# Performance work log

Hardware: AMD Instinct MI355X
Metric: run time of the kernel (lower is better)

Reference implementation:

```python
import jax, jax.numpy as jnp
import numpy as np

B, S, D, H, DF = 512, 256, 256, 8, 1024
DA, DZ, DO = 64, 64, 128
NA, NZ, NO = 9, 20, 7


def _pe(b, s):
    # Faithful to the torch code: zeros_like(src) is 3D, so 'seq_len'=batch,
    # 'd_model'=seq; pos_encoding[pos, i] assigns whole feature rows.
    pos = jnp.arange(b, dtype=jnp.float32)[:, None]
    i = jnp.arange(s, dtype=jnp.float32)[None, :]
    ang = pos / jnp.power(100.0, 2.0 * i / s)
    pe = jnp.where((jnp.arange(s)[None, :] % 2) == 0, jnp.sin(ang), jnp.cos(ang))
    return pe[:, :, None]  # broadcasts over feature dim


def _ln(x, g, b):
    m = x.mean(-1, keepdims=True)
    v = x.var(-1, keepdims=True)
    return (x - m) / jnp.sqrt(v + 1e-5) * g + b


def _lin(x, w, b):
    return x @ w.T + b


def _forward(X, emb_act_w, emb_zone_w, lin0_w, lin0_b, qkv_w, qkv_b, attn_o_w, attn_o_b,
             ln1_g, ln1_b, ff1_w, ff1_b, ff2_w, ff2_b, ln2_g, ln2_b,
             relu_w, relu_b, dT_w, dT_b, lindT_w, lindT_b, zn_w, zn_b,
             linzn_w, linzn_b, act0_w, act0_b, act1_w, act1_b, linact_w, linact_b):
    a = X[:, :, 0]
    z = X[:, :, 1]
    o = X[:, :, 2:].astype(jnp.float32)
    x = jnp.concatenate([emb_act_w[a], emb_zone_w[z], _lin(o, lin0_w, lin0_b)], -1)
    src = x + _pe(x.shape[0], x.shape[1])
    # TransformerEncoderLayer: post-norm, relu FFN, eval (dropout off)
    qkv = _lin(src, qkv_w, qkv_b)
    q, k, v = jnp.split(qkv, 3, -1)
    hd = D // H
    q = q.reshape(q.shape[0], q.shape[1], H, hd)
    k = k.reshape(k.shape[0], k.shape[1], H, hd)
    v = v.reshape(v.shape[0], v.shape[1], H, hd)
    sc = jnp.einsum('bqhd,bkhd->bhqk', q, k) * (float(hd) ** -0.5)
    att = jax.nn.softmax(sc, -1)
    ao = jnp.einsum('bhqk,bkhd->bqhd', att, v).reshape(src.shape)
    h1 = _ln(src + _lin(ao, attn_o_w, attn_o_b), ln1_g, ln1_b)
    h2 = _ln(h1 + _lin(jax.nn.relu(_lin(h1, ff1_w, ff1_b)), ff2_w, ff2_b), ln2_g, ln2_b)
    x_relu = _lin(h2[:, -1, :], relu_w, relu_b)  # NOTE: no relu in original
    dT = _lin(_lin(x_relu, dT_w, dT_b), lindT_w, lindT_b)  # [B,1]
    zn = _lin(_lin(jnp.concatenate([dT, x_relu], 1), zn_w, zn_b), linzn_w, linzn_b)  # [B,20]
    fa = jnp.concatenate([zn, dT, x_relu], 1)  # [B,277]
    ac = _lin(_lin(_lin(fa, act0_w, act0_b), act1_w, act1_b), linact_w, linact_b)  # [B,5]
    return jnp.concatenate([dT, zn, ac], 1)  # [B,26]


def setup_inputs() -> dict:
    ks = jax.random.split(jax.random.key(0), 24)

    def p(k, shape):
        return jax.random.normal(k, shape, jnp.float32) * 0.02

    inp = {
        'X': jax.random.randint(ks[0], (B, S, 2 + NO), 0, NA).astype(jnp.int32),
        'emb_act_w': p(ks[1], (NA, DA)),
        'emb_zone_w': p(ks[2], (NZ, DZ)),
        'lin0_w': p(ks[3], (DO, NO)), 'lin0_b': jnp.zeros((DO,), jnp.float32),
        'qkv_w': p(ks[4], (3 * D, D)), 'qkv_b': jnp.zeros((3 * D,), jnp.float32),
        'attn_o_w': p(ks[5], (D, D)), 'attn_o_b': jnp.zeros((D,), jnp.float32),
        'ln1_g': jnp.ones((D,), jnp.float32), 'ln1_b': jnp.zeros((D,), jnp.float32),
        'ff1_w': p(ks[6], (DF, D)), 'ff1_b': jnp.zeros((DF,), jnp.float32),
        'ff2_w': p(ks[7], (D, DF)), 'ff2_b': jnp.zeros((D,), jnp.float32),
        'ln2_g': jnp.ones((D,), jnp.float32), 'ln2_b': jnp.zeros((D,), jnp.float32),
        'relu_w': p(ks[8], (D, D)), 'relu_b': jnp.zeros((D,), jnp.float32),
        'dT_w': p(ks[9], (D, D)), 'dT_b': jnp.zeros((D,), jnp.float32),
        'lindT_w': p(ks[10], (1, D)), 'lindT_b': jnp.zeros((1,), jnp.float32),
        'zn_w': p(ks[11], (D + 1, D + 1)), 'zn_b': jnp.zeros((D + 1,), jnp.float32),
        'linzn_w': p(ks[12], (20, D + 1)), 'linzn_b': jnp.zeros((20,), jnp.float32),
        'act0_w': p(ks[13], (D + 21, D + 21)), 'act0_b': jnp.zeros((D + 21,), jnp.float32),
        'act1_w': p(ks[14], (D + 21, D + 21)), 'act1_b': jnp.zeros((D + 21,), jnp.float32),
        'linact_w': p(ks[15], (5, D + 21)), 'linact_b': jnp.zeros((5,), jnp.float32),
    }
    return inp


def reference(X, emb_act_w, emb_zone_w, lin0_w, lin0_b, qkv_w, qkv_b, attn_o_w, attn_o_b,
              ln1_g, ln1_b, ff1_w, ff1_b, ff2_w, ff2_b, ln2_g, ln2_b,
              relu_w, relu_b, dT_w, dT_b, lindT_w, lindT_b, zn_w, zn_b,
              linzn_w, linzn_b, act0_w, act0_b, act1_w, act1_b, linact_w, linact_b):
    return _forward(X, emb_act_w, emb_zone_w, lin0_w, lin0_b, qkv_w, qkv_b, attn_o_w, attn_o_b,
                    ln1_g, ln1_b, ff1_w, ff1_b, ff2_w, ff2_b, ln2_g, ln2_b,
                    relu_w, relu_b, dT_w, dT_b, lindT_w, lindT_b, zn_w, zn_b,
                    linzn_w, linzn_b, act0_w, act0_b, act1_w, act1_b, linact_w, linact_b)
```

## Files before the change

kernel.cpp:

```cpp
#include <hip/hip_runtime.h>
#include <math.h>

#define BATCH 512
#define SEQ   256
#define DIM   256
#define NHEAD 8
#define DFF   1024
#define NT    1024
#define NW    16

typedef unsigned short ushort;
typedef unsigned int   uint;
typedef __fp16 half2v __attribute__((ext_vector_type(2)));

#define OFF_QKV   0u
#define OFF_AO    196608u
#define OFF_FF1   262144u
#define OFF_FF2   524288u
#define OFF_RELU  786432u
#define OFF_DT    851968u
#define OFF_ZN    917504u
#define OFF_A0    983553u
#define OFF_A1    1060282u
#define OFF_KT    1137011u
#define CVT_TOTAL 1202547u

__global__ __launch_bounds__(512) void cvt_weights(
    const float* __restrict__ qkv, const float* __restrict__ ao,
    const float* __restrict__ ff1, const float* __restrict__ ff2,
    const float* __restrict__ relu, const float* __restrict__ dT,
    const float* __restrict__ zn, const float* __restrict__ a0,
    const float* __restrict__ a1, ushort* __restrict__ ws) {
  uint i = blockIdx.x * 512u + threadIdx.x;
  if (i >= CVT_TOTAL) return;
  float v;
  if (i >= OFF_KT) {
    uint idx = i - OFF_KT;
    uint d = idx >> 8, k = idx & 255u;
    v = qkv[(size_t)(256 + k) * 256 + d];
  } else {
    const float* src; uint off;
    if      (i < OFF_AO)  { src = qkv;  off = OFF_QKV; }
    else if (i < OFF_FF1) { src = ao;   off = OFF_AO; }
    else if (i < OFF_FF2) { src = ff1;  off = OFF_FF1; }
    else if (i < OFF_RELU){ src = ff2;  off = OFF_FF2; }
    else if (i < OFF_DT)  { src = relu; off = OFF_RELU; }
    else if (i < OFF_ZN)  { src = dT;   off = OFF_DT; }
    else if (i < OFF_A0)  { src = zn;   off = OFF_ZN; }
    else if (i < OFF_A1)  { src = a0;   off = OFF_A0; }
    else                  { src = a1;   off = OFF_A1; }
    v = src[i - off];
  }
  __fp16 h = (__fp16)v;
  union { __fp16 h; ushort u; } c; c.h = h;
  ws[i] = c.u;
}


__device__ __forceinline__ half2v u2h(uint u) {
  union { uint u; half2v h; } c; c.u = u; return c.h;
}

__device__ __forceinline__ float wave_allred(float v) {
  #pragma unroll
  for (int off = 32; off > 0; off >>= 1) v += __shfl_xor(v, off, 64);
  return v;
}

__device__ __forceinline__ float fold4(int lane, float p0, float p1, float p2, float p3) {
  float za = (lane & 32) ? p1 : p0;
  float ta = (lane & 32) ? p0 : p1;
  za += __shfl_xor(ta, 32, 64);
  float zb = (lane & 32) ? p3 : p2;
  float tb = (lane & 32) ? p2 : p3;
  zb += __shfl_xor(tb, 32, 64);
  float u = (lane & 16) ? zb : za;
  float t = (lane & 16) ? za : zb;
  u += __shfl_xor(t, 16, 64);
  u += __shfl_xor(u, 8, 64);
  u += __shfl_xor(u, 4, 64);
  u += __shfl_xor(u, 2, 64);
  u += __shfl_xor(u, 1, 64);
  return u;
}

__device__ __forceinline__ float fold4h(int lane, const float p[4]) {
  float z0 = (lane & 16) ? p[1] : p[0], y0 = (lane & 16) ? p[0] : p[1];
  z0 += __shfl_xor(y0, 16, 64);
  float z1 = (lane & 16) ? p[3] : p[2], y1 = (lane & 16) ? p[2] : p[3];
  z1 += __shfl_xor(y1, 16, 64);
  float u = (lane & 8) ? z1 : z0, t = (lane & 8) ? z0 : z1;
  u += __shfl_xor(t, 8, 64);
  u += __shfl_xor(u, 4, 64);
  u += __shfl_xor(u, 2, 64);
  u += __shfl_xor(u, 1, 64);
  return u;
}

__device__ __forceinline__ bool burst_writer4(int lane, int& row_off) {
  if (lane & 7) return false;
  int g = (lane >> 3) & 3;
  int iv = ((g & 1) << 1) | ((g >> 1) & 1);
  row_off = ((lane >> 5) << 2) + iv;
  return true;
}

struct XH { half2v h[4]; };

__device__ __forceinline__ XH ldx8h(const float* __restrict__ x, int lane) {
  int k = (lane & 31) * 8;
  XH r;
  r.h[0] = __builtin_amdgcn_cvt_pkrtz(x[k],     x[k + 1]);
  r.h[1] = __builtin_amdgcn_cvt_pkrtz(x[k + 2], x[k + 3]);
  r.h[2] = __builtin_amdgcn_cvt_pkrtz(x[k + 4], x[k + 5]);
  r.h[3] = __builtin_amdgcn_cvt_pkrtz(x[k + 6], x[k + 7]);
  return r;
}

__device__ __forceinline__ void accum1(uint4 w, const XH& x, float& p) {
  p = __builtin_amdgcn_fdot2(u2h(w.x), x.h[0], p, false);
  p = __builtin_amdgcn_fdot2(u2h(w.y), x.h[1], p, false);
  p = __builtin_amdgcn_fdot2(u2h(w.z), x.h[2], p, false);
  p = __builtin_amdgcn_fdot2(u2h(w.w), x.h[3], p, false);
}

struct W4 { uint4 w[4]; };

__device__ __forceinline__ W4 ldw4(const ushort* __restrict__ Wb, int ld, int lane) {
  const ushort* wp = Wb + (size_t)((lane >> 5) * 4) * ld + (lane & 31) * 8;
  W4 r;
  #pragma unroll
  for (int i = 0; i < 4; ++i) r.w[i] = *(const uint4*)(wp + (size_t)i * ld);
  return r;
}

__device__ __forceinline__ void accum4(const W4& w, const XH& x, float p[4]) {
  #pragma unroll
  for (int i = 0; i < 4; ++i) accum1(w.w[i], x, p[i]);
}

__device__ __forceinline__ float block_sum16(float v, float* red) {
  #pragma unroll
  for (int off = 32; off > 0; off >>= 1) v += __shfl_xor(v, off, 64);
  __syncthreads();
  if ((threadIdx.x & 63) == 0) red[threadIdx.x >> 6] = v;
  __syncthreads();
  float s = 0.f;
  #pragma unroll
  for (int i = 0; i < NW; ++i) s += red[i];
  return s;
}

struct Buf {
  float sc[2048];
  float pe[SEQ];
  float srcl[DIM];
  float qv[DIM];
  float ao[DIM];
  float h1[DIM];
  float h2[DIM];
  float xr[DIM];
  float znin[260];
  float fa[280];
  float znv[20];
  float cb[8];
  float scA[9 * 8];
  float scZ[20 * 8];
  float mHJ[8 * 8];
  float biasO8[8];
  float wsum8[8];
  float attA[8 * 9];
  float attZ[8 * 20];
  float oAcc[8 * 7];
  float peAcc8[8];
  int   Xa[SEQ];
  int   Xz[SEQ];
  float Xo[SEQ * 7];
};


__global__ __launch_bounds__(NT, 8) void nmstpp_fused(
    const int*   __restrict__ X,
    const float* __restrict__ emb_act,
    const float* __restrict__ emb_zone,
    const float* __restrict__ lin0_w,
    const float* __restrict__ lin0_b,
    const ushort* __restrict__ w16,
    const float* __restrict__ qkv_b,
    const float* __restrict__ attn_o_b,
    const float* __restrict__ ln1_g, const float* __restrict__ ln1_b,
    const float* __restrict__ ff1_b,
    const float* __restrict__ ff2_b,
    const float* __restrict__ ln2_g, const float* __restrict__ ln2_b,
    const float* __restrict__ relu_b,
    const float* __restrict__ dT_b,
    const float* __restrict__ lindT_w,
    const float* __restrict__ lindT_b,
    const float* __restrict__ zn_b,
    const float* __restrict__ linzn_w,
    const float* __restrict__ linzn_b,
    const float* __restrict__ act0_b,
    const float* __restrict__ act1_b,
    const float* __restrict__ linact_w,
    const float* __restrict__ linact_b,
    float* __restrict__ out)
{
  const int tid  = threadIdx.x;
  const int wid  = tid >> 6;
  const int lane = tid & 63;
  const int b    = blockIdx.x;
  const int hq2  = (tid >> 8) * 2;
  const int dd   = tid & 255;

  const ushort* qkv16  = w16 + OFF_QKV;
  const ushort* ao16   = w16 + OFF_AO;
  const ushort* ff116  = w16 + OFF_FF1;
  const ushort* ff216  = w16 + OFF_FF2;
  const ushort* relu16 = w16 + OFF_RELU;
  const ushort* dT16   = w16 + OFF_DT;
  const ushort* kt16   = w16 + OFF_KT;
  const __fp16* znh  = (const __fp16*)(w16 + OFF_ZN);
  const __fp16* a0h  = (const __fp16*)(w16 + OFF_A0);
  const __fp16* a1h  = (const __fp16*)(w16 + OFF_A1);

  __shared__ alignas(16) Buf s;
  __shared__ float embA[9 * 65];
  __shared__ float embZ[20 * 65];
  __shared__ float l0w[128 * 7];
  __shared__ float l0b[128];
  __shared__ float red[NW];

  for (int i = tid; i < 9 * 64;  i += NT) embA[(i >> 6) * 65 + (i & 63)] = emb_act[i];
  for (int i = tid; i < 20 * 64; i += NT) embZ[(i >> 6) * 65 + (i & 63)] = emb_zone[i];
  for (int i = tid; i < 128 * 7; i += NT) l0w[i] = lin0_w[i];
  if (tid < 128) l0b[tid] = lin0_b[tid];
  if (tid < SEQ) {
    const int* xrow = X + (b * SEQ + tid) * 9;
    s.Xa[tid] = xrow[0];
    s.Xz[tid] = xrow[1];
    #pragma unroll
    for (int j = 0; j < 7; ++j) s.Xo[tid * 7 + j] = (float)xrow[2 + j];
    float ex  = (float)(2 * tid) / (float)SEQ;
    float ang = (float)b * exp2f(-ex * 6.643856189774724f);
    s.pe[tid] = ((tid & 1) == 0) ? __sinf(ang) : __cosf(ang);
  }
  __syncthreads();

  if (tid < DIM) {
    int av = s.Xa[SEQ - 1], zv = s.Xz[SEQ - 1];
    float v;
    if (tid < 64)        v = embA[av * 65 + tid];
    else if (tid < 128)  v = embZ[zv * 65 + (tid - 64)];
    else {
      const float* lr = l0w + (tid - 128) * 7;
      float acc = l0b[tid - 128];
      #pragma unroll
      for (int j = 0; j < 7; ++j) acc = fmaf(lr[j], s.Xo[(SEQ - 1) * 7 + j], acc);
      v = acc;
    }
    s.srcl[tid] = v + s.pe[SEQ - 1];
  }
  __syncthreads();

  {
    XH x = ldx8h(s.srcl, lane);
    #pragma unroll 1
    for (int t = 0; t < 2; ++t) {
      int base = (wid + 16 * t) * 8;
      W4 w = ldw4(qkv16 + (size_t)base * 256, 256, lane);
      float p[4] = {};
      accum4(w, x, p);
      float u = fold4h(lane, p);
      int ro;
      if (burst_writer4(lane, ro)) s.qv[base + ro] = qkv_b[base + ro] + u;
    }
  }
  __syncthreads();

  {
    XH x = ldx8h(s.qv, lane);
    const float inv = 0.17677669529663687f;
    #pragma unroll 1
    for (int t = 0; t < 2; ++t) {
      int base = (wid + 16 * t) * 8;
      W4 w = ldw4(kt16 + (size_t)base * 256, 256, lane);
      float p[4] = {};
      accum4(w, x, p);
      #pragma unroll
      for (int i = 0; i < 4; ++i) {
        p[i] += __shfl_xor(p[i], 1, 4);
        p[i] += __shfl_xor(p[i], 2, 4);
      }
      int sub = lane & 31;
      int h = sub >> 2, jj = sub & 3;
      int dbase = base + ((lane >> 5) << 2);
      s.sc[(dbase + jj) * 8 + h] = p[jj] * inv;
    }
  }
  __syncthreads();

  if (tid < 312) {
    if (tid < 296) {
      int h = tid / 37, k = tid - h * 37;
      if (k < 9) {
        float acc = 0.f;
        for (int c = 0; c < 64; ++c) acc = fmaf(s.sc[c * 8 + h], embA[k * 65 + c], acc);
        s.scA[k * 8 + h] = acc;
      } else if (k < 29) {
        int z = k - 9; float acc = 0.f;
        for (int c = 0; c < 64; ++c) acc = fmaf(s.sc[(64 + c) * 8 + h], embZ[z * 65 + c], acc);
        s.scZ[z * 8 + h] = acc;
      } else if (k < 36) {
        int j = k - 29; float acc = 0.f;
        for (int kk = 0; kk < 128; ++kk) acc = fmaf(s.sc[(128 + kk) * 8 + h], l0w[kk * 7 + j], acc);
        s.mHJ[h * 8 + j] = acc;
      } else {
        float acc = 0.f;
        for (int c = 0; c < 256; ++c) acc += s.sc[c * 8 + h];
        s.wsum8[h] = acc;
      }
    } else if (tid < 304) {
      int h = tid - 296; float acc = 0.f;
      for (int kk = 0; kk < 128; ++kk) acc = fmaf(s.sc[(128 + kk) * 8 + h], l0b[kk], acc);
      s.biasO8[h] = acc;
    } else {
      int h = tid - 304; float acc = 0.f;
      for (int c = 0; c < 32; ++c) acc += s.qv[h * 32 + c] * qkv_b[DIM + h * 32 + c];
      s.cb[h] = acc * 0.17677669529663687f;
    }
  }
  __syncthreads();

  {
    const int sp = dd;
    int av = s.Xa[sp], zv = s.Xz[sp];
    float o[7];
    #pragma unroll
    for (int j = 0; j < 7; ++j) o[j] = s.Xo[sp * 7 + j];
    float pes = s.pe[sp];
    #pragma unroll
    for (int hh = 0; hh < 2; ++hh) {
      int h = hq2 + hh;
      float acc = s.scA[av * 8 + h] + s.scZ[zv * 8 + h] + s.biasO8[h] + s.cb[h];
      acc = fmaf(pes, s.wsum8[h], acc);
      #pragma unroll
      for (int j = 0; j < 7; ++j) acc = fmaf(s.mHJ[h * 8 + j], o[j], acc);
      s.sc[h * SEQ + sp] = acc;
    }
  }
  __syncthreads();

  {
    const bool act = (wid < 8);
    const int h = wid & 7;
    float vals[4]; float rinv = 0.f;
    if (act) {
      float m = -1e30f;
      #pragma unroll
      for (int i = 0; i < 4; ++i) {
        vals[i] = s.sc[h * SEQ + lane * 4 + i];
        m = fmaxf(m, vals[i]);
      }
      #pragma unroll
      for (int off = 32; off > 0; off >>= 1) m = fmaxf(m, __shfl_xor(m, off, 64));
      float lsum = 0.f;
      #pragma unroll
      for (int i = 0; i < 4; ++i) { vals[i] = __expf(vals[i] - m); lsum += vals[i]; }
      #pragma unroll
      for (int off = 32; off > 0; off >>= 1) lsum += __shfl_xor(lsum, off, 64);
      rinv = 1.0f / lsum;
    }
    __syncthreads();
    if (act) {
      #pragma unroll
      for (int i = 0; i < 4; ++i) s.sc[(lane * 4 + i) * 8 + h] = vals[i] * rinv;
    }
  }
  __syncthreads();

  if (wid < 8) {
    const int h = wid;
    float att[4];
    #pragma unroll
    for (int i = 0; i < 4; ++i) att[i] = s.sc[(lane + 64 * i) * 8 + h];
    {
      float v = 0.f;
      #pragma unroll
      for (int i = 0; i < 4; ++i) v = fmaf(att[i], s.pe[lane + 64 * i], v);
      v = wave_allred(v);
      if (lane == 0) s.peAcc8[h] = v;
    }
    #pragma unroll
    for (int j = 0; j < 7; ++j) {
      float v = 0.f;
      #pragma unroll
      for (int i = 0; i < 4; ++i) v = fmaf(att[i], s.Xo[(lane + 64 * i) * 7 + j], v);
      v = wave_allred(v);
      if (lane == 0) s.oAcc[h * 7 + j] = v;
    }
    int code[4];
    #pragma unroll
    for (int i = 0; i < 4; ++i) {
      int sp = lane + 64 * i;
      code[i] = s.Xa[sp] | (s.Xz[sp] << 8);
    }
    for (int a = 0; a < 9; ++a) {
      float v = 0.f;
      #pragma unroll
      for (int i = 0; i < 4; ++i) v += ((code[i] & 255) == a) ? att[i] : 0.f;
      v = wave_allred(v);
      if (lane == 0) s.attA[h * 9 + a] = v;
    }
    for (int z = 0; z < 20; ++z) {
      float v = 0.f;
      #pragma unroll
      for (int i = 0; i < 4; ++i) v += ((code[i] >> 8) == z) ? att[i] : 0.f;
      v = wave_allred(v);
      if (lane == 0) s.attZ[h * 20 + z] = v;
    }
  }
  __syncthreads();

  {
    float acc[2];
    #pragma unroll
    for (int hh = 0; hh < 2; ++hh) acc[hh] = s.peAcc8[hq2 + hh];
    if (dd < 64) {
      for (int a = 0; a < 9; ++a) {
        float ev = embA[a * 65 + dd];
        #pragma unroll
        for (int hh = 0; hh < 2; ++hh) acc[hh] = fmaf(s.attA[(hq2 + hh) * 9 + a], ev, acc[hh]);
      }
    } else if (dd < 128) {
      int d2 = dd - 64;
      for (int z = 0; z < 20; ++z) {
        float ev = embZ[z * 65 + d2];
        #pragma unroll
        for (int hh = 0; hh < 2; ++hh) acc[hh] = fmaf(s.attZ[(hq2 + hh) * 20 + z], ev, acc[hh]);
      }
    } else {
      int kk = dd - 128;
      #pragma unroll
      for (int j = 0; j < 7; ++j) {
        float ov = l0w[kk * 7 + j];
        #pragma unroll
        for (int hh = 0; hh < 2; ++hh) acc[hh] = fmaf(s.oAcc[(hq2 + hh) * 7 + j], ov, acc[hh]);
      }
      #pragma unroll
      for (int hh = 0; hh < 2; ++hh) acc[hh] += l0b[kk];
    }
    #pragma unroll
    for (int hh = 0; hh < 2; ++hh) s.sc[(hq2 + hh) * DIM + dd] = acc[hh];
  }
  __syncthreads();

  {
    #pragma unroll 1
    for (int t = 0; t < 2; ++t) {
      int rb = wid + 16 * t;
      int base = rb * 8;
      XH x = ldx8h(s.sc + (rb >> 2) * DIM, lane);
      W4 w = ldw4(qkv16 + (size_t)(2 * DIM + base) * 256, 256, lane);
      float p[4] = {};
      accum4(w, x, p);
      float u = fold4h(lane, p);
      int ro;
      if (burst_writer4(lane, ro)) s.ao[base + ro] = qkv_b[2 * DIM + base + ro] + u;
    }
  }
  __syncthreads();

  {
    XH x = ldx8h(s.ao, lane);
    #pragma unroll 1
    for (int t = 0; t < 2; ++t) {
      int base = (wid + 16 * t) * 8;
      W4 w = ldw4(ao16 + (size_t)base * 256, 256, lane);
      float p[4] = {};
      accum4(w, x, p);
      float u = fold4h(lane, p);
      int ro;
      if (burst_writer4(lane, ro)) {
        int rr = base + ro;
        s.qv[rr] = s.srcl[rr] + attn_o_b[rr] + u;
      }
    }
  }
  __syncthreads();
  {
    float tv = (tid < DIM) ? s.qv[tid] : 0.f;
    float mean = block_sum16(tv, red) * (1.0f / 256.0f);
    float dv = (tid < DIM) ? (tv - mean) : 0.f;
    float var = block_sum16(dv * dv, red) * (1.0f / 256.0f);
    if (tid < DIM) s.h1[tid] = dv / sqrtf(var + 1e-5f) * ln1_g[tid] + ln1_b[tid];
  }
  __syncthreads();

  {
    XH x = ldx8h(s.h1, lane);
    #pragma unroll 1
    for (int t = 0; t < 8; ++t) {
      int base = (wid + 16 * t) * 8;
      W4 w = ldw4(ff116 + (size_t)base * 256, 256, lane);
      float p[4] = {};
      accum4(w, x, p);
      float u = fold4h(lane, p);
      int ro;
      if (burst_writer4(lane, ro)) {
        int rr = base + ro;
        s.sc[rr] = fmaxf(ff1_b[rr] + u, 0.f);
      }
    }
  }
  __syncthreads();

  {
    #pragma unroll 1
    for (int t = 0; t < 2; ++t) {
      int base = (wid + 16 * t) * 8;
      float p[4] = {};
      #pragma unroll 1
      for (int kc = 0; kc < 4; ++kc) {
        XH x = ldx8h(s.sc + kc * 256, lane);
        W4 w = ldw4(ff216 + (size_t)base * 1024 + kc * 256, 1024, lane);
        accum4(w, x, p);
      }
      float u = fold4h(lane, p);
      int ro;
      if (burst_writer4(lane, ro)) {
        int rr = base + ro;
        s.qv[rr] = s.h1[rr] + ff2_b[rr] + u;
      }
    }
  }
  __syncthreads();
  {
    float tv = (tid < DIM) ? s.qv[tid] : 0.f;
    float mean = block_sum16(tv, red) * (1.0f / 256.0f);
    float dv = (tid < DIM) ? (tv - mean) : 0.f;
    float var = block_sum16(dv * dv, red) * (1.0f / 256.0f);
    if (tid < DIM) s.h2[tid] = dv / sqrtf(var + 1e-5f) * ln2_g[tid] + ln2_b[tid];
  }
  __syncthreads();

  {
    XH x = ldx8h(s.h2, lane);
    #pragma unroll 1
    for (int t = 0; t < 2; ++t) {
      int base = (wid + 16 * t) * 8;
      W4 w = ldw4(relu16 + (size_t)base * 256, 256, lane);
      float p[4] = {};
      accum4(w, x, p);
      float u = fold4h(lane, p);
      int ro;
      if (burst_writer4(lane, ro)) s.xr[base + ro] = relu_b[base + ro] + u;
    }
  }
  __syncthreads();

  {
    XH x = ldx8h(s.xr, lane);
    #pragma unroll 1
    for (int t = 0; t < 2; ++t) {
      int base = (wid + 16 * t) * 8;
      W4 w = ldw4(dT16 + (size_t)base * 256, 256, lane);
      float p[4] = {};
      accum4(w, x, p);
      float u = fold4h(lane, p);
      int ro;
      if (burst_writer4(lane, ro)) s.h1[base + ro] = dT_b[base + ro] + u;
    }
  }
  __syncthreads();
  float dTv;
  {
    float v = (tid < DIM) ? lindT_w[tid] * s.h1[tid] : 0.f;
    dTv = block_sum16(v, red) + lindT_b[0];
  }

  if (tid < DIM) { s.znin[1 + tid] = s.xr[tid]; s.fa[21 + tid] = s.xr[tid]; }
  if (tid == 0)  { s.znin[0] = dTv; s.fa[20] = dTv; }
  __syncthreads();
  float* z1 = s.sc + 1024;
  for (int r0 = 4 * wid; r0 < 257; r0 += 4 * NW) {
    int nrow = 257 - r0; if (nrow > 4) nrow = 4;
    float p0 = 0, p1 = 0, p2 = 0, p3 = 0;
    for (int j = lane; j < 257; j += 64) {
      float xv = s.znin[j];
      const __fp16* wp = znh + (size_t)r0 * 257 + j;
      p0 = fmaf((float)wp[0], xv, p0);
      if (nrow > 1) p1 = fmaf((float)wp[257], xv, p1);
      if (nrow > 2) p2 = fmaf((float)wp[2 * 257], xv, p2);
      if (nrow > 3) p3 = fmaf((float)wp[3 * 257], xv, p3);
    }
    float u = fold4(lane, p0, p1, p2, p3);
    if ((lane & 15) == 0) {
      int g = lane >> 4;
      int rr = r0 + ((g & 1) << 1) + (g >> 1);
      if (rr < 257) z1[rr] = zn_b[rr] + u;
    }
  }
  __syncthreads();
  for (int r0 = 4 * wid; r0 < 20; r0 += 4 * NW) {
    float p0 = 0, p1 = 0, p2 = 0, p3 = 0;
    for (int j = lane; j < 257; j += 64) {
      float xv = z1[j];
      const float* wp = linzn_w + (size_t)r0 * 257 + j;
      p0 = fmaf(wp[0], xv, p0);
      p1 = fmaf(wp[257], xv, p1);
      p2 = fmaf(wp[2 * 257], xv, p2);
      p3 = fmaf(wp[3 * 257], xv, p3);
    }
    float u = fold4(lane, p0, p1, p2, p3);
    if ((lane & 15) == 0) {
      int g = lane >> 4;
      int rr = r0 + ((g & 1) << 1) + (g >> 1);
      if (rr < 20) { float v = linzn_b[rr] + u; s.znv[rr] = v; s.fa[rr] = v; }
    }
  }
  __syncthreads();

  float* a0v = s.sc + 1312;
  for (int r0 = 4 * wid; r0 < 277; r0 += 4 * NW) {
    int nrow = 277 - r0; if (nrow > 4) nrow = 4;
    float p0 = 0, p1 = 0, p2 = 0, p3 = 0;
    for (int j = lane; j < 277; j += 64) {
      float xv = s.fa[j];
      const __fp16* wp = a0h + (size_t)r0 * 277 + j;
      p0 = fmaf((float)wp[0], xv, p0);
      if (nrow > 1) p1 = fmaf((float)wp[277], xv, p1);
      if (nrow > 2) p2 = fmaf((float)wp[2 * 277], xv, p2);
      if (nrow > 3) p3 = fmaf((float)wp[3 * 277], xv, p3);
    }
    float u = fold4(lane, p0, p1, p2, p3);
    if ((lane & 15) == 0) {
      int g = lane >> 4;
      int rr = r0 + ((g & 1) << 1) + (g >> 1);
      if (rr < 277) a0v[rr] = act0_b[rr] + u;
    }
  }
  __syncthreads();
  float* a1v = s.sc + 1024;
  for (int r0 = 4 * wid; r0 < 277; r0 += 4 * NW) {
    int nrow = 277 - r0; if (nrow > 4) nrow = 4;
    float p0 = 0, p1 = 0, p2 = 0, p3 = 0;
    for (int j = lane; j < 277; j += 64) {
      float xv = a0v[j];
      const __fp16* wp = a1h + (size_t)r0 * 277 + j;
      p0 = fmaf((float)wp[0], xv, p0);
      if (nrow > 1) p1 = fmaf((float)wp[277], xv, p1);
      if (nrow > 2) p2 = fmaf((float)wp[2 * 277], xv, p2);
      if (nrow > 3) p3 = fmaf((float)wp[3 * 277], xv, p3);
    }
    float u = fold4(lane, p0, p1, p2, p3);
    if ((lane & 15) == 0) {
      int g = lane >> 4;
      int rr = r0 + ((g & 1) << 1) + (g >> 1);
      if (rr < 277) a1v[rr] = act1_b[rr] + u;
    }
  }
  __syncthreads();

  if (wid < 5) {
    const float* wr = linact_w + (size_t)wid * 277;
    float p = 0.f;
    for (int j = lane; j < 277; j += 64) p = fmaf(wr[j], a1v[j], p);
    #pragma unroll
    for (int off = 32; off > 0; off >>= 1) p += __shfl_xor(p, off, 64);
    if (lane == 0) out[b * 26 + 21 + wid] = linact_b[wid] + p;
  }
  if (tid == 0) out[b * 26] = dTv;
  if (tid < 20) out[b * 26 + 1 + tid] = s.znv[tid];
}


extern "C" void kernel_launch(void* const* d_in, const int* in_sizes, int n_in,
                              void* d_out, int out_size, void* d_ws, size_t ws_size,
                              hipStream_t stream) {
  (void)in_sizes; (void)n_in; (void)out_size; (void)ws_size;
  const int*   X        = (const int*)  d_in[0];
  const float* emb_act  = (const float*)d_in[1];
  const float* emb_zone = (const float*)d_in[2];
  const float* lin0_w   = (const float*)d_in[3];
  const float* lin0_b   = (const float*)d_in[4];
  const float* qkv_w    = (const float*)d_in[5];
  const float* qkv_b    = (const float*)d_in[6];
  const float* attn_o_w = (const float*)d_in[7];
  const float* attn_o_b = (const float*)d_in[8];
  const float* ln1_g    = (const float*)d_in[9];
  const float* ln1_b    = (const float*)d_in[10];
  const float* ff1_w    = (const float*)d_in[11];
  const float* ff1_b    = (const float*)d_in[12];
  const float* ff2_w    = (const float*)d_in[13];
  const float* ff2_b    = (const float*)d_in[14];
  const float* ln2_g    = (const float*)d_in[15];
  const float* ln2_b    = (const float*)d_in[16];
  const float* relu_w   = (const float*)d_in[17];
  const float* relu_b   = (const float*)d_in[18];
  const float* dT_w     = (const float*)d_in[19];
  const float* dT_b     = (const float*)d_in[20];
  const float* lindT_w  = (const float*)d_in[21];
  const float* lindT_b  = (const float*)d_in[22];
  const float* zn_w     = (const float*)d_in[23];
  const float* zn_b     = (const float*)d_in[24];
  const float* linzn_w  = (const float*)d_in[25];
  const float* linzn_b  = (const float*)d_in[26];
  const float* act0_w   = (const float*)d_in[27];
  const float* act0_b   = (const float*)d_in[28];
  const float* act1_w   = (const float*)d_in[29];
  const float* act1_b   = (const float*)d_in[30];
  const float* linact_w = (const float*)d_in[31];
  const float* linact_b = (const float*)d_in[32];
  float* out = (float*)d_out;
  ushort* w16 = (ushort*)d_ws;

  cvt_weights<<<dim3((CVT_TOTAL + 511) / 512), dim3(512), 0, stream>>>(
      qkv_w, attn_o_w, ff1_w, ff2_w, relu_w, dT_w, zn_w, act0_w, act1_w, w16);

  nmstpp_fused<<<dim3(BATCH), dim3(NT), 0, stream>>>(
      X, emb_act, emb_zone, lin0_w, lin0_b, w16, qkv_b, attn_o_b,
      ln1_g, ln1_b, ff1_b, ff2_b, ln2_g, ln2_b,
      relu_b, dT_b, lindT_w, lindT_b, zn_b,
      linzn_w, linzn_b, act0_b, act1_b, linact_w, linact_b,
      out);
}
```

Before: 133.2 us.

## Halve block size to 512 threads and compact per-block input staging

Shrinks each workgroup from 1024 to 512 threads (8 waves). Every GEMV loop now runs twice as many iterations per wave, and the per-head loops handle four heads per thread instead of two. The softmax and attention stages drop their idle-wave guards because all 8 waves now map to the 8 heads. Action and zone indices are packed into one int and the observation features are stored as fp16 in shared memory, and LayerNorm computes mean and sum-of-squares in a single fused reduction. The aim is fewer idle waves, cheaper barriers and less shared memory, at the cost of less latency hiding per block and a one-pass variance that is less numerically stable.

```diff
diff --git a/kernel.cpp b/kernel.cpp
--- a/kernel.cpp
+++ b/kernel.cpp
@@ -6,8 +6,8 @@
 #define DIM   256
 #define NHEAD 8
 #define DFF   1024
-#define NT    1024
-#define NW    16
+#define NT    512
+#define NW    8
 
 typedef unsigned short ushort;
 typedef unsigned int   uint;
@@ -139,7 +139,7 @@
   for (int i = 0; i < 4; ++i) accum1(w.w[i], x, p[i]);
 }
 
-__device__ __forceinline__ float block_sum16(float v, float* red) {
+__device__ __forceinline__ float block_sum8(float v, float* red) {
   #pragma unroll
   for (int off = 32; off > 0; off >>= 1) v += __shfl_xor(v, off, 64);
   __syncthreads();
@@ -149,6 +149,24 @@
   #pragma unroll
   for (int i = 0; i < NW; ++i) s += red[i];
   return s;
+}
+
+__device__ __forceinline__ void block_sum8x2(float a, float b2, float* red,
+                                             float& A, float& B) {
+  #pragma unroll
+  for (int off = 32; off > 0; off >>= 1) {
+    a  += __shfl_xor(a,  off, 64);
+    b2 += __shfl_xor(b2, off, 64);
+  }
+  __syncthreads();
+  if ((threadIdx.x & 63) == 0) {
+    red[threadIdx.x >> 6] = a;
+    red[NW + (threadIdx.x >> 6)] = b2;
+  }
+  __syncthreads();
+  A = 0.f; B = 0.f;
+  #pragma unroll
+  for (int i = 0; i < NW; ++i) { A += red[i]; B += red[NW + i]; }
 }
 
 struct Buf {
@@ -173,9 +191,8 @@
   float attZ[8 * 20];
   float oAcc[8 * 7];
   float peAcc8[8];
-  int   Xa[SEQ];
-  int   Xz[SEQ];
-  float Xo[SEQ * 7];
+  int    Xcode[SEQ];
+  __fp16 Xoh[SEQ * 7];
 };
 
 
@@ -209,7 +226,7 @@
   const int wid  = tid >> 6;
   const int lane = tid & 63;
   const int b    = blockIdx.x;
-  const int hq2  = (tid >> 8) * 2;
+  const int hb4  = (tid >> 8) * 4;
   const int dd   = tid & 255;
 
   const ushort* qkv16  = w16 + OFF_QKV;
@@ -228,7 +245,7 @@
   __shared__ float embZ[20 * 65];
   __shared__ float l0w[128 * 7];
   __shared__ float l0b[128];
-  __shared__ float red[NW];
+  __shared__ float red[2 * NW];
 
   for (int i = tid; i < 9 * 64;  i += NT) embA[(i >> 6) * 65 + (i & 63)] = emb_act[i];
   for (int i = tid; i < 20 * 64; i += NT) embZ[(i >> 6) * 65 + (i & 63)] = emb_zone[i];
@@ -236,10 +253,9 @@
   if (tid < 128) l0b[tid] = lin0_b[tid];
   if (tid < SEQ) {
     const int* xrow = X + (b * SEQ + tid) * 9;
-    s.Xa[tid] = xrow[0];
-    s.Xz[tid] = xrow[1];
-    #pragma unroll
-    for (int j = 0; j < 7; ++j) s.Xo[tid * 7 + j] = (float)xrow[2 + j];
+    s.Xcode[tid] = xrow[0] | (xrow[1] << 8);
+    #pragma unroll
+    for (int j = 0; j < 7; ++j) s.Xoh[tid * 7 + j] = (__fp16)(float)xrow[2 + j];
     float ex  = (float)(2 * tid) / (float)SEQ;
     float ang = (float)b * exp2f(-ex * 6.643856189774724f);
     s.pe[tid] = ((tid & 1) == 0) ? __sinf(ang) : __cosf(ang);
@@ -247,7 +263,8 @@
   __syncthreads();
 
   if (tid < DIM) {
-    int av = s.Xa[SEQ - 1], zv = s.Xz[SEQ - 1];
+    int code = s.Xcode[SEQ - 1];
+    int av = code & 255, zv = code >> 8;
     float v;
     if (tid < 64)        v = embA[av * 65 + tid];
     else if (tid < 128)  v = embZ[zv * 65 + (tid - 64)];
@@ -255,7 +272,7 @@
       const float* lr = l0w + (tid - 128) * 7;
       float acc = l0b[tid - 128];
       #pragma unroll
-      for (int j = 0; j < 7; ++j) acc = fmaf(lr[j], s.Xo[(SEQ - 1) * 7 + j], acc);
+      for (int j = 0; j < 7; ++j) acc = fmaf(lr[j], (float)s.Xoh[(SEQ - 1) * 7 + j], acc);
       v = acc;
     }
     s.srcl[tid] = v + s.pe[SEQ - 1];
@@ -265,8 +282,8 @@
   {
     XH x = ldx8h(s.srcl, lane);
     #pragma unroll 1
-    for (int t = 0; t < 2; ++t) {
-      int base = (wid + 16 * t) * 8;
+    for (int t = 0; t < 4; ++t) {
+      int base = (wid + 8 * t) * 8;
       W4 w = ldw4(qkv16 + (size_t)base * 256, 256, lane);
       float p[4] = {};
       accum4(w, x, p);
@@ -281,8 +298,8 @@
     XH x = ldx8h(s.qv, lane);
     const float inv = 0.17677669529663687f;
     #pragma unroll 1
-    for (int t = 0; t < 2; ++t) {
-      int base = (wid + 16 * t) * 8;
+    for (int t = 0; t < 4; ++t) {
+      int base = (wid + 8 * t) * 8;
       W4 w = ldw4(kt16 + (size_t)base * 256, 256, lane);
       float p[4] = {};
       accum4(w, x, p);
@@ -333,14 +350,15 @@
 
   {
     const int sp = dd;
-    int av = s.Xa[sp], zv = s.Xz[sp];
+    int code = s.Xcode[sp];
+    int av = code & 255, zv = code >> 8;
     float o[7];
     #pragma unroll
-    for (int j = 0; j < 7; ++j) o[j] = s.Xo[sp * 7 + j];
+    for (int j = 0; j < 7; ++j) o[j] = (float)s.Xoh[sp * 7 + j];
     float pes = s.pe[sp];
     #pragma unroll
-    for (int hh = 0; hh < 2; ++hh) {
-      int h = hq2 + hh;
+    for (int hh = 0; hh < 4; ++hh) {
+      int h = hb4 + hh;
       float acc = s.scA[av * 8 + h] + s.scZ[zv * 8 + h] + s.biasO8[h] + s.cb[h];
       acc = fmaf(pes, s.wsum8[h], acc);
       #pragma unroll
@@ -351,34 +369,29 @@
   __syncthreads();
 
   {
-    const bool act = (wid < 8);
-    const int h = wid & 7;
-    float vals[4]; float rinv = 0.f;
-    if (act) {
-      float m = -1e30f;
-      #pragma unroll
-      for (int i = 0; i < 4; ++i) {
-        vals[i] = s.sc[h * SEQ + lane * 4 + i];
-        m = fmaxf(m, vals[i]);
-      }
-      #pragma unroll
-      for (int off = 32; off > 0; off >>= 1) m = fmaxf(m, __shfl_xor(m, off, 64));
-      float lsum = 0.f;
-      #pragma unroll
-      for (int i = 0; i < 4; ++i) { vals[i] = __expf(vals[i] - m); lsum += vals[i]; }
-      #pragma unroll
-      for (int off = 32; off > 0; off >>= 1) lsum += __shfl_xor(lsum, off, 64);
-      rinv = 1.0f / lsum;
-    }
+    const int h = wid;
+    float vals[4];
+    float m = -1e30f;
+    #pragma unroll
+    for (int i = 0; i < 4; ++i) {
+      vals[i] = s.sc[h * SEQ + lane * 4 + i];
+      m = fmaxf(m, vals[i]);
+    }
+    #pragma unroll
+    for (int off = 32; off > 0; off >>= 1) m = fmaxf(m, __shfl_xor(m, off, 64));
+    float lsum = 0.f;
+    #pragma unroll
+    for (int i = 0; i < 4; ++i) { vals[i] = __expf(vals[i] - m); lsum += vals[i]; }
+    #pragma unroll
+    for (int off = 32; off > 0; off >>= 1) lsum += __shfl_xor(lsum, off, 64);
+    float rinv = 1.0f / lsum;
     __syncthreads();
-    if (act) {
-      #pragma unroll
-      for (int i = 0; i < 4; ++i) s.sc[(lane * 4 + i) * 8 + h] = vals[i] * rinv;
-    }
-  }
-  __syncthreads();
-
-  if (wid < 8) {
+    #pragma unroll
+    for (int i = 0; i < 4; ++i) s.sc[(lane * 4 + i) * 8 + h] = vals[i] * rinv;
+  }
+  __syncthreads();
+
+  {
     const int h = wid;
     float att[4];
     #pragma unroll
@@ -394,16 +407,13 @@
     for (int j = 0; j < 7; ++j) {
       float v = 0.f;
       #pragma unroll
-      for (int i = 0; i < 4; ++i) v = fmaf(att[i], s.Xo[(lane + 64 * i) * 7 + j], v);
+      for (int i = 0; i < 4; ++i) v = fmaf(att[i], (float)s.Xoh[(lane + 64 * i) * 7 + j], v);
       v = wave_allred(v);
       if (lane == 0) s.oAcc[h * 7 + j] = v;
     }
     int code[4];
     #pragma unroll
-    for (int i = 0; i < 4; ++i) {
-      int sp = lane + 64 * i;
-      code[i] = s.Xa[sp] | (s.Xz[sp] << 8);
-    }
+    for (int i = 0; i < 4; ++i) code[i] = s.Xcode[lane + 64 * i];
     for (int a = 0; a < 9; ++a) {
       float v = 0.f;
       #pragma unroll
@@ -422,21 +432,21 @@
   __syncthreads();
 
   {
-    float acc[2];
-    #pragma unroll
-    for (int hh = 0; hh < 2; ++hh) acc[hh] = s.peAcc8[hq2 + hh];
+    float acc[4];
+    #pragma unroll
+    for (int hh = 0; hh < 4; ++hh) acc[hh] = s.peAcc8[hb4 + hh];
     if (dd < 64) {
       for (int a = 0; a < 9; ++a) {
         float ev = embA[a * 65 + dd];
         #pragma unroll
-        for (int hh = 0; hh < 2; ++hh) acc[hh] = fmaf(s.attA[(hq2 + hh) * 9 + a], ev, acc[hh]);
+        for (int hh = 0; hh < 4; ++hh) acc[hh] = fmaf(s.attA[(hb4 + hh) * 9 + a], ev, acc[hh]);
       }
     } else if (dd < 128) {
       int d2 = dd - 64;
       for (int z = 0; z < 20; ++z) {
         float ev = embZ[z * 65 + d2];
         #pragma unroll
-        for (int hh = 0; hh < 2; ++hh) acc[hh] = fmaf(s.attZ[(hq2 + hh) * 20 + z], ev, acc[hh]);
+        for (int hh = 0; hh < 4; ++hh) acc[hh] = fmaf(s.attZ[(hb4 + hh) * 20 + z], ev, acc[hh]);
       }
     } else {
       int kk = dd - 128;
@@ -444,20 +454,20 @@
       for (int j = 0; j < 7; ++j) {
         float ov = l0w[kk * 7 + j];
         #pragma unroll
-        for (int hh = 0; hh < 2; ++hh) acc[hh] = fmaf(s.oAcc[(hq2 + hh) * 7 + j], ov, acc[hh]);
-      }
-      #pragma unroll
-      for (int hh = 0; hh < 2; ++hh) acc[hh] += l0b[kk];
-    }
-    #pragma unroll
-    for (int hh = 0; hh < 2; ++hh) s.sc[(hq2 + hh) * DIM + dd] = acc[hh];
+        for (int hh = 0; hh < 4; ++hh) acc[hh] = fmaf(s.oAcc[(hb4 + hh) * 7 + j], ov, acc[hh]);
+      }
+      #pragma unroll
+      for (int hh = 0; hh < 4; ++hh) acc[hh] += l0b[kk];
+    }
+    #pragma unroll
+    for (int hh = 0; hh < 4; ++hh) s.sc[(hb4 + hh) * DIM + dd] = acc[hh];
   }
   __syncthreads();
 
   {
     #pragma unroll 1
-    for (int t = 0; t < 2; ++t) {
-      int rb = wid + 16 * t;
+    for (int t = 0; t < 4; ++t) {
+      int rb = wid + 8 * t;
       int base = rb * 8;
       XH x = ldx8h(s.sc + (rb >> 2) * DIM, lane);
       W4 w = ldw4(qkv16 + (size_t)(2 * DIM + base) * 256, 256, lane);
@@ -473,8 +483,8 @@
   {
     XH x = ldx8h(s.ao, lane);
     #pragma unroll 1
-    for (int t = 0; t < 2; ++t) {
-      int base = (wid + 16 * t) * 8;
+    for (int t = 0; t < 4; ++t) {
+      int base = (wid + 8 * t) * 8;
       W4 w = ldw4(ao16 + (size_t)base * 256, 256, lane);
       float p[4] = {};
       accum4(w, x, p);
@@ -489,18 +499,19 @@
   __syncthreads();
   {
     float tv = (tid < DIM) ? s.qv[tid] : 0.f;
-    float mean = block_sum16(tv, red) * (1.0f / 256.0f);
-    float dv = (tid < DIM) ? (tv - mean) : 0.f;
-    float var = block_sum16(dv * dv, red) * (1.0f / 256.0f);
-    if (tid < DIM) s.h1[tid] = dv / sqrtf(var + 1e-5f) * ln1_g[tid] + ln1_b[tid];
+    float A, B;
+    block_sum8x2(tv, tv * tv, red, A, B);
+    float mean = A * (1.0f / 256.0f);
+    float var = B * (1.0f / 256.0f) - mean * mean;
+    if (tid < DIM) s.h1[tid] = (tv - mean) / sqrtf(var + 1e-5f) * ln1_g[tid] + ln1_b[tid];
   }
   __syncthreads();
 
   {
     XH x = ldx8h(s.h1, lane);
     #pragma unroll 1
-    for (int t = 0; t < 8; ++t) {
-      int base = (wid + 16 * t) * 8;
+    for (int t = 0; t < 16; ++t) {
+      int base = (wid + 8 * t) * 8;
       W4 w = ldw4(ff116 + (size_t)base * 256, 256, lane);
       float p[4] = {};
       accum4(w, x, p);
@@ -516,8 +527,8 @@
 
   {
     #pragma unroll 1
-    for (int t = 0; t < 2; ++t) {
-      int base = (wid + 16 * t) * 8;
+    for (int t = 0; t < 4; ++t) {
+      int base = (wid + 8 * t) * 8;
       float p[4] = {};
       #pragma unroll 1
       for (int kc = 0; kc < 4; ++kc) {
@@ -536,18 +547,19 @@
   __syncthreads();
   {
     float tv = (tid < DIM) ? s.qv[tid] : 0.f;
-    float mean = block_sum16(tv, red) * (1.0f / 256.0f);
-    float dv = (tid < DIM) ? (tv - mean) : 0.f;
-    float var = block_sum16(dv * dv, red) * (1.0f / 256.0f);
-    if (tid < DIM) s.h2[tid] = dv / sqrtf(var + 1e-5f) * ln2_g[tid] + ln2_b[tid];
+    float A, B;
+    block_sum8x2(tv, tv * tv, red, A, B);
+    float mean = A * (1.0f / 256.0f);
+    float var = B * (1.0f / 256.0f) - mean * mean;
+    if (tid < DIM) s.h2[tid] = (tv - mean) / sqrtf(var + 1e-5f) * ln2_g[tid] + ln2_b[tid];
   }
   __syncthreads();
 
   {
     XH x = ldx8h(s.h2, lane);
     #pragma unroll 1
-    for (int t = 0; t < 2; ++t) {
-      int base = (wid + 16 * t) * 8;
+    for (int t = 0; t < 4; ++t) {
+      int base = (wid + 8 * t) * 8;
       W4 w = ldw4(relu16 + (size_t)base * 256, 256, lane);
       float p[4] = {};
       accum4(w, x, p);
@@ -561,8 +573,8 @@
   {
     XH x = ldx8h(s.xr, lane);
     #pragma unroll 1
-    for (int t = 0; t < 2; ++t) {
-      int base = (wid + 16 * t) * 8;
+    for (int t = 0; t < 4; ++t) {
+      int base = (wid + 8 * t) * 8;
       W4 w = ldw4(dT16 + (size_t)base * 256, 256, lane);
       float p[4] = {};
       accum4(w, x, p);
@@ -575,7 +587,7 @@
   float dTv;
   {
     float v = (tid < DIM) ? lindT_w[tid] * s.h1[tid] : 0.f;
-    dTv = block_sum16(v, red) + lindT_b[0];
+    dTv = block_sum8(v, red) + lindT_b[0];
   }
 
   if (tid < DIM) { s.znin[1 + tid] = s.xr[tid]; s.fa[21 + tid] = s.xr[tid]; }
```

Measured after the change: 194.1 us. 1.46x slower.
